# Performance work log

Hardware: AMD Instinct MI355X
Metric: run time of the kernel (lower is better)

Reference implementation:

```python
import jax, jax.numpy as jnp
import numpy as np

B, C, H, W = 4, 512, 64, 64
CQ = C // 8  # 64 channels for each of query/key projections


def conv1x1(t, w, b):
    # t: [B, Cin, H, W], w: [Cout, Cin], b: [Cout]
    return jnp.einsum('bchw,oc->bohw', t, w) + b[None, :, None, None]


def setup_inputs() -> dict:
    key = jax.random.key(0)
    ks = jax.random.split(key, 12)
    s = 0.05
    return {
        'x':   jax.random.normal(ks[0], (B, C, H, W), jnp.float32),
        'dep': jax.random.normal(ks[1], (B, C, H, W), jnp.float32),
        'wq':  jax.random.normal(ks[2], (CQ, C), jnp.float32) * s,
        'bq':  jnp.zeros((CQ,), jnp.float32),
        'wqd': jax.random.normal(ks[3], (CQ, C), jnp.float32) * s,
        'bqd': jnp.zeros((CQ,), jnp.float32),
        'wk':  jax.random.normal(ks[4], (CQ, C), jnp.float32) * s,
        'bk':  jnp.zeros((CQ,), jnp.float32),
        'wkd': jax.random.normal(ks[5], (CQ, C), jnp.float32) * s,
        'bkd': jnp.zeros((CQ,), jnp.float32),
        'wv':  jax.random.normal(ks[6], (C, C), jnp.float32) * s,
        'bv':  jnp.zeros((C,), jnp.float32),
        'gamma': jnp.full((1,), 0.5, jnp.float32),
    }


def reference(x, dep, wq, bq, wqd, bqd, wk, bk, wkd, bkd, wv, bv, gamma):
    b, c, h, w = x.shape
    n = h * w
    # concatenated RGB+depth query/key projections: [B, 2*CQ, N]
    q = jnp.concatenate([conv1x1(x, wq, bq), conv1x1(dep, wqd, bqd)], axis=1).reshape(b, -1, n)
    k = jnp.concatenate([conv1x1(x, wk, bk), conv1x1(dep, wkd, bkd)], axis=1).reshape(b, -1, n)
    # energy[b, i, j] = sum_d q[b, d, i] * k[b, d, j]  -> [B, N, N]
    energy = jnp.einsum('bdi,bdj->bij', q, k)
    attn = jax.nn.softmax(energy, axis=-1)
    v = conv1x1(x, wv, bv).reshape(b, c, n)  # [B, C, N]
    # out[b, c, i] = sum_j v[b, c, j] * attn[b, i, j]
    out = jnp.einsum('bcj,bij->bci', v, attn).reshape(b, c, h, w)
    return gamma.reshape(()) * out + x
```

## Files before the change

kernel.cpp:

```cpp
#include <hip/hip_runtime.h>


typedef __attribute__((ext_vector_type(8))) short bf16x8;
typedef __attribute__((ext_vector_type(4))) float f32x4;

__device__ __forceinline__ float bf2f(unsigned short u) {
  return __builtin_bit_cast(float, (unsigned int)u << 16);
}
__device__ __forceinline__ unsigned short f2bf(float f) {
  unsigned int u = __builtin_bit_cast(unsigned int, f);
  u = u + 0x7fffu + ((u >> 16) & 1u);
  return (unsigned short)(u >> 16);
}
__device__ __forceinline__ float bflo(unsigned int u) {
  return __builtin_bit_cast(float, u << 16);
}

__device__ __forceinline__ void gld16(const char* g, char* l) {
  __builtin_amdgcn_global_load_lds(
      (const __attribute__((address_space(1))) unsigned int*)g,
      (__attribute__((address_space(3))) unsigned int*)l, 16, 0, 0);
}

__device__ __forceinline__ int detect_fp32_mode(const void* xv) {
  const unsigned int* p = (const unsigned int*)xv;
  const int lane = threadIdx.x & 63;
  const unsigned int w0 = p[lane];
  const unsigned int w1 = p[64 + lane];
  int cnt = 0;
  const unsigned short us[4] = {
      (unsigned short)(w0 & 0xffffu), (unsigned short)(w0 >> 16),
      (unsigned short)(w1 & 0xffffu), (unsigned short)(w1 >> 16)};
#pragma unroll
  for (int h = 0; h < 4; ++h) {
    const float a = fabsf(bf2f(us[h]));
    cnt += (a > 9.0e-13f && a < 32.0f) ? 1 : 0;
  }
#pragma unroll
  for (int mm = 32; mm >= 1; mm >>= 1) cnt += __shfl_xor(cnt, mm, 64);
  return cnt < 220;
}

__global__ __launch_bounds__(256) void prep_kernel(
    const void* wq, const void* bq, const void* wqd, const void* bqd,
    const void* wk, const void* bk, const void* wkd, const void* bkd,
    const void* wv, const void* bv, const void* gam, const void* x,
    unsigned short* __restrict__ Whi, unsigned short* __restrict__ Wlo,
    float* __restrict__ Bcat, float* __restrict__ gamF)
{
  const int fp32mode = detect_fp32_mode(x);
  const int row = blockIdx.x;
  const void* src; const void* bsrc; int srow;
  if (row < 64)       { src = wq;  bsrc = bq;  srow = row; }
  else if (row < 128) { src = wqd; bsrc = bqd; srow = row - 64; }
  else if (row < 192) { src = wk;  bsrc = bk;  srow = row - 128; }
  else if (row < 256) { src = wkd; bsrc = bkd; srow = row - 192; }
  else                { src = wv;  bsrc = bv;  srow = row - 256; }
  for (int c = threadIdx.x; c < 512; c += 256) {
    const float v = fp32mode ? ((const float*)src)[(size_t)srow * 512 + c]
                             : bf2f(((const unsigned short*)src)[(size_t)srow * 512 + c]);
    const unsigned short h = f2bf(v);
    Whi[(size_t)row * 512 + c] = h;
    Wlo[(size_t)row * 512 + c] = f2bf(v - bf2f(h));
  }
  if (threadIdx.x == 0) {
    Bcat[row] = fp32mode ? ((const float*)bsrc)[srow]
                         : bf2f(((const unsigned short*)bsrc)[srow]);
    if (row == 0)
      gamF[0] = fp32mode ? ((const float*)gam)[0]
                         : bf2f(((const unsigned short*)gam)[0]);
  }
}

__device__ __forceinline__ void stage_X(
    const void* __restrict__ src, int fp32mode, int b, int n0,
    int cbase, int nn,
    unsigned short* __restrict__ Xhi, unsigned short* __restrict__ Xlo)
{
  float v[8][4];
  if (fp32mode) {
    const float* s = (const float*)src;
#pragma unroll
    for (int r = 0; r < 8; ++r) {
      const int c = cbase + r * 64;
      const float4 f4 = *(const float4*)(s + (((size_t)b * 512 + c) << 12) + n0 + nn);
      v[r][0] = f4.x; v[r][1] = f4.y; v[r][2] = f4.z; v[r][3] = f4.w;
    }
  } else {
    const unsigned short* s = (const unsigned short*)src;
#pragma unroll
    for (int r = 0; r < 8; ++r) {
      const int c = cbase + r * 64;
      const uint2 u2 = *(const uint2*)(s + (((size_t)b * 512 + c) << 12) + n0 + nn);
      v[r][0] = bflo(u2.x & 0xffffu); v[r][1] = bflo(u2.x >> 16);
      v[r][2] = bflo(u2.y & 0xffffu); v[r][3] = bflo(u2.y >> 16);
    }
  }
  __builtin_amdgcn_sched_barrier(0);
#pragma unroll
  for (int r = 0; r < 8; ++r) {
    const int c = cbase + r * 64;
#pragma unroll
    for (int k = 0; k < 4; ++k) {
      const unsigned short h = f2bf(v[r][k]);
      Xhi[(nn + k) * 522 + c] = h;
      Xlo[(nn + k) * 522 + c] = f2bf(v[r][k] - bf2f(h));
    }
  }
}

__device__ __forceinline__ void do_tile_c(
    const unsigned short* __restrict__ Whi, const unsigned short* __restrict__ Wlo,
    const float* bsh,
    const unsigned short* Xhi, const unsigned short* Xlo, int fp32mode,
    int wrow0, int kind, int d0,
    int l15, int quad,
    char* __restrict__ QT, char* __restrict__ KT, char* __restrict__ VT)
{
  f32x4 A0, A1, B0, B1, C0, C1;
#pragma unroll
  for (int r = 0; r < 4; ++r) {
    A0[r] = A1[r] = bsh[wrow0 + quad * 4 + r];
    B0[r] = B1[r] = C0[r] = C1[r] = 0.f;
  }
  const unsigned short* wh_p = Whi + (size_t)(wrow0 + l15) * 512 + quad * 8;
  const unsigned short* wl_p = Wlo + (size_t)(wrow0 + l15) * 512 + quad * 8;
  const unsigned short* x0h = Xhi + l15 * 522 + quad * 8;
  const unsigned short* x1h = Xhi + (16 + l15) * 522 + quad * 8;
  const unsigned short* x0l = Xlo + l15 * 522 + quad * 8;
  const unsigned short* x1l = Xlo + (16 + l15) * 522 + quad * 8;

  bf16x8 hc = *(const bf16x8*)(wh_p);
  bf16x8 lc;
  if (fp32mode) lc = *(const bf16x8*)(wl_p);

#pragma unroll 2
  for (int ks = 0; ks < 16; ++ks) {
    bf16x8 hn, ln;
    if (ks < 15) {
      hn = *(const bf16x8*)(wh_p + (ks + 1) * 32);
      if (fp32mode) ln = *(const bf16x8*)(wl_p + (ks + 1) * 32);
    }
    const int o = ks * 32;
    const bf16x8 b0 = *(const bf16x8*)(x0h + o);
    const bf16x8 b1 = *(const bf16x8*)(x1h + o);
    A0 = __builtin_amdgcn_mfma_f32_16x16x32_bf16(hc, b0, A0, 0, 0, 0);
    A1 = __builtin_amdgcn_mfma_f32_16x16x32_bf16(hc, b1, A1, 0, 0, 0);
    if (fp32mode) {
      const bf16x8 c0 = *(const bf16x8*)(x0l + o);
      const bf16x8 c1 = *(const bf16x8*)(x1l + o);
      B0 = __builtin_amdgcn_mfma_f32_16x16x32_bf16(hc, c0, B0, 0, 0, 0);
      C0 = __builtin_amdgcn_mfma_f32_16x16x32_bf16(lc, b0, C0, 0, 0, 0);
      B1 = __builtin_amdgcn_mfma_f32_16x16x32_bf16(hc, c1, B1, 0, 0, 0);
      C1 = __builtin_amdgcn_mfma_f32_16x16x32_bf16(lc, b1, C1, 0, 0, 0);
    }
    if (ks < 15) { hc = hn; if (fp32mode) lc = ln; }
  }

  const f32x4 a0 = fp32mode ? (A0 + B0) + C0 : A0;
  const f32x4 a1 = fp32mode ? (A1 + B1) + C1 : A1;
#pragma unroll
  for (int ns = 0; ns < 2; ++ns) {
    const f32x4 acc = ns ? a1 : a0;
    const int n = ns * 16 + l15;
    if (kind <= 1) {
      ushort4 h, l;
#pragma unroll
      for (int r = 0; r < 4; ++r) {
        const float f = acc[r];
        const unsigned short hh = f2bf(f);
        ((unsigned short*)&h)[r] = hh;
        ((unsigned short*)&l)[r] = f2bf(f - bf2f(hh));
      }
      const unsigned lin = (unsigned)(n * 256 + (d0 + quad * 4) * 2);
      if (kind == 0) {
        *(ushort4*)(QT + lin) = h;
        *(ushort4*)(QT + 8192 + lin) = l;
      } else {
        const unsigned off = lin ^ ((unsigned)(n & 7) << 4);
        *(ushort4*)(KT + off) = h;
        *(ushort4*)(KT + 8192 + off) = l;
      }
    } else {
#pragma unroll
      for (int r = 0; r < 4; ++r) {
        const int c = d0 + quad * 4 + r;
        const unsigned off =
            ((unsigned)(c * 64 + n * 2)) ^ ((unsigned)(c & 7) << 4);
        *(unsigned short*)(VT + off) = f2bf(acc[r]);
      }
    }
  }
}

__global__ __launch_bounds__(512, 2) void proj_kernel(
    const void* __restrict__ x, const void* __restrict__ dep,
    const unsigned short* __restrict__ Whi, const unsigned short* __restrict__ Wlo,
    const float* __restrict__ Bcat,
    unsigned short* __restrict__ Qhi, unsigned short* __restrict__ Qlo,
    unsigned short* __restrict__ Kst, unsigned short* __restrict__ Vst)
{
  __shared__ unsigned short Xhi[32 * 522];
  __shared__ unsigned short Xlo[32 * 522];
  __shared__ char QT[16384];
  __shared__ char KT[16384];
  __shared__ char VT[32768];
  __shared__ float bsh[768];
  const int fp32mode = detect_fp32_mode(x);
  const int tid  = threadIdx.x;
  const int lane = tid & 63;
  const int w    = tid >> 6;
  const int l15  = lane & 15;
  const int quad = lane >> 4;
  const int b  = blockIdx.y;

  const int cbase = tid >> 3;
  const int nn    = (tid & 7) * 4;

  for (int i = tid; i < 768; i += 512) bsh[i] = Bcat[i];

  for (int rep = 0; rep < 2; ++rep) {
    const int t  = blockIdx.x + rep * 64;
    const int n0 = t * 32;

    stage_X(x, fp32mode, b, n0, cbase, nn, Xhi, Xlo);
    __syncthreads();

    for (int rt = w; rt < 40; rt += 8) {
      int wrow0, kind, d0;
      if (rt < 4)      { wrow0 = rt * 16;             kind = 0; d0 = rt * 16; }
      else if (rt < 8) { wrow0 = 128 + (rt - 4) * 16; kind = 1; d0 = (rt - 4) * 16; }
      else             { wrow0 = 256 + (rt - 8) * 16; kind = 2; d0 = (rt - 8) * 16; }
      do_tile_c(Whi, Wlo, bsh, Xhi, Xlo, fp32mode, wrow0, kind, d0,
                l15, quad, QT, KT, VT);
    }
    __syncthreads();

    {
      char* vdst = (char*)Vst + (((size_t)b * 128 + t) << 15);
#pragma unroll
      for (int i = 0; i < 4; ++i) {
        const int off = i * 8192 + tid * 16;
        *(uint4*)(vdst + off) = *(const uint4*)(VT + off);
      }
    }
    stage_X(dep, fp32mode, b, n0, cbase, nn, Xhi, Xlo);
    __syncthreads();

    {
      const int rt = w;
      const int kind  = (rt < 4) ? 0 : 1;
      const int wrow0 = (rt < 4) ? 64 + rt * 16 : 192 + (rt - 4) * 16;
      const int d0    = 64 + (rt & 3) * 16;
      do_tile_c(Whi, Wlo, bsh, Xhi, Xlo, fp32mode, wrow0, kind, d0,
                l15, quad, QT, KT, VT);
    }
    __syncthreads();

    {
      char* kdst = (char*)Kst + (((size_t)b * 128 + t) << 14);
#pragma unroll
      for (int i = 0; i < 2; ++i) {
        const int off = i * 8192 + tid * 16;
        *(uint4*)(kdst + off) = *(const uint4*)(KT + off);
      }
      const size_t qoff = ((((size_t)b << 12) + n0) * 128) * 2;
      *(uint4*)((char*)Qhi + qoff + tid * 16) = *(const uint4*)(QT + tid * 16);
      *(uint4*)((char*)Qlo + qoff + tid * 16) = *(const uint4*)(QT + 8192 + tid * 16);
    }
    __syncthreads();
  }
}

__global__ __launch_bounds__(768, 3) void attn_kernel(
    const unsigned short* __restrict__ Qhi, const unsigned short* __restrict__ Qlo,
    const unsigned short* __restrict__ Kst, const unsigned short* __restrict__ Vst,
    const void* __restrict__ x, const float* __restrict__ gamF,
    void* __restrict__ outp)
{
  __shared__ char KL[2][16384];
  __shared__ char VL[2][32768];
  __shared__ unsigned short P[2][64][40];
  __shared__ float lstat[2][4][16];

  const int fp32mode = detect_fp32_mode(x);
  const int tid  = threadIdx.x;
  const int lane = tid & 63;
  const int w    = tid >> 6;
  const int l15  = lane & 15;
  const int quad = lane >> 4;
  const int id   = blockIdx.x;
  const int b    = (id >> 1) & 3;
  const int n0   = (((id >> 3) << 1) | (id & 1)) * 64;

  asm volatile("" :: "v"(fp32mode) : "memory");

  const char* Kb = (const char*)Kst + (((size_t)b * 128) << 14);
  const char* Vb = (const char*)Vst + (((size_t)b * 128) << 15);

  if (w < 4) {
    const int ihE = w >> 1;
    const int jt  = w & 1;
    bf16x8 qh[2][4], ql[2][4];
#pragma unroll
    for (int itq = 0; itq < 2; ++itq) {
      const size_t qb =
          (((size_t)b << 12) + n0 + ihE * 32 + itq * 16 + l15) * 128 + quad * 8;
#pragma unroll
      for (int ds = 0; ds < 4; ++ds) {
        qh[itq][ds] = *(const bf16x8*)(Qhi + qb + ds * 32);
        ql[itq][ds] = *(const bf16x8*)(Qlo + qb + ds * 32);
      }
    }
#pragma unroll
    for (int ch = 0; ch < 4; ++ch) {
      const int c = w + ch * 4;
      gld16(Kb + c * 1024 + lane * 16, &KL[0][c * 1024]);
    }
    float lpart[2] = {0.f, 0.f};

    for (int t = 0; t <= 128; ++t) {
      asm volatile("s_waitcnt vmcnt(0) lgkmcnt(0)" ::: "memory");
      __builtin_amdgcn_sched_barrier(0);
      __builtin_amdgcn_s_barrier();
      __builtin_amdgcn_sched_barrier(0);
      if (t < 128) {
        const int cur = t & 1;
        if (t < 127) {
          const char* src = Kb + ((size_t)(t + 1) << 14);
#pragma unroll
          for (int ch = 0; ch < 4; ++ch) {
            const int c = w + ch * 4;
            gld16(src + c * 1024 + lane * 16, &KL[cur ^ 1][c * 1024]);
          }
        }
        __builtin_amdgcn_sched_barrier(0);
        const int row = jt * 16 + l15;
        const unsigned rsw = (unsigned)(row & 7) << 4;
        const char* kb = &KL[cur][0];
        bf16x8 kh[4], kl[4];
#pragma unroll
        for (int ds = 0; ds < 4; ++ds) {
          const unsigned off = ((unsigned)(row * 256 + quad * 16 + ds * 64)) ^ rsw;
          kh[ds] = *(const bf16x8*)(kb + off);
          kl[ds] = *(const bf16x8*)(kb + 8192 + off);
        }
        f32x4 ea[2], eb[2], ec[2];
#pragma unroll
        for (int itq = 0; itq < 2; ++itq) {
          ea[itq] = (f32x4){0.f, 0.f, 0.f, 0.f};
          eb[itq] = (f32x4){0.f, 0.f, 0.f, 0.f};
          ec[itq] = (f32x4){0.f, 0.f, 0.f, 0.f};
        }
        __builtin_amdgcn_s_setprio(1);
#pragma unroll
        for (int ds = 0; ds < 4; ++ds)
#pragma unroll
          for (int itq = 0; itq < 2; ++itq) {
            ea[itq] = __builtin_amdgcn_mfma_f32_16x16x32_bf16(kh[ds], qh[itq][ds], ea[itq], 0, 0, 0);
            eb[itq] = __builtin_amdgcn_mfma_f32_16x16x32_bf16(kh[ds], ql[itq][ds], eb[itq], 0, 0, 0);
            ec[itq] = __builtin_amdgcn_mfma_f32_16x16x32_bf16(kl[ds], qh[itq][ds], ec[itq], 0, 0, 0);
          }
        __builtin_amdgcn_s_setprio(0);
#pragma unroll
        for (int itq = 0; itq < 2; ++itq) {
          const f32x4 e = (ea[itq] + eb[itq]) + ec[itq];
          const float p0 = __expf(e[0] - 32.0f);
          const float p1 = __expf(e[1] - 32.0f);
          const float p2 = __expf(e[2] - 32.0f);
          const float p3 = __expf(e[3] - 32.0f);
          const unsigned short u0 = f2bf(p0), u1 = f2bf(p1);
          const unsigned short u2 = f2bf(p2), u3 = f2bf(p3);
          lpart[itq] += (bf2f(u0) + bf2f(u1)) + (bf2f(u2) + bf2f(u3));
          unsigned int* dst = (unsigned int*)
              (&P[cur][ihE * 32 + itq * 16 + l15][jt * 16 + quad * 4]);
          dst[0] = (unsigned int)u0 | ((unsigned int)u1 << 16);
          dst[1] = (unsigned int)u2 | ((unsigned int)u3 << 16);
        }
      }
    }
#pragma unroll
    for (int itq = 0; itq < 2; ++itq) {
      float lp = lpart[itq];
      lp += __shfl_xor(lp, 16, 64);
      lp += __shfl_xor(lp, 32, 64);
      if (quad == 0) lstat[jt][ihE * 2 + itq][l15] = lp;
    }
    __syncthreads();
    return;
  }

  const int wv = w - 4;
#pragma unroll
  for (int k = 0; k < 4; ++k) {
    const int c = wv * 4 + k;
    gld16(Vb + c * 1024 + lane * 16, &VL[0][c * 1024]);
  }
  f32x4 acc[4][4];
#pragma unroll
  for (int ct = 0; ct < 4; ++ct)
#pragma unroll
    for (int itv = 0; itv < 4; ++itv) acc[ct][itv] = (f32x4){0.f, 0.f, 0.f, 0.f};

  for (int t = 0; t <= 128; ++t) {
    if (t <= 127)
      asm volatile("s_waitcnt vmcnt(4)" ::: "memory");
    else
      asm volatile("s_waitcnt vmcnt(0)" ::: "memory");
    __builtin_amdgcn_sched_barrier(0);
    __builtin_amdgcn_s_barrier();
    __builtin_amdgcn_sched_barrier(0);
    if (t >= 1) {
      const int pb = (t - 1) & 1;
      bf16x8 pf[4];
#pragma unroll
      for (int itv = 0; itv < 4; ++itv)
        pf[itv] = *(const bf16x8*)(&P[pb][itv * 16 + l15][quad * 8]);
      const char* vb = &VL[pb][0];
      __builtin_amdgcn_s_setprio(1);
#pragma unroll
      for (int ct = 0; ct < 4; ++ct) {
        const int c = wv * 64 + ct * 16 + l15;
        const unsigned off =
            ((unsigned)(c * 64 + quad * 16)) ^ ((unsigned)(c & 7) << 4);
        const bf16x8 va = *(const bf16x8*)(vb + off);
#pragma unroll
        for (int itv = 0; itv < 4; ++itv)
          acc[ct][itv] = __builtin_amdgcn_mfma_f32_16x16x32_bf16(va, pf[itv], acc[ct][itv], 0, 0, 0);
      }
      __builtin_amdgcn_s_setprio(0);
      __builtin_amdgcn_sched_barrier(0);
    }
    if (t < 127) {
      const char* src = Vb + ((size_t)(t + 1) << 15);
#pragma unroll
      for (int k = 0; k < 4; ++k) {
        const int c = wv * 4 + k;
        gld16(src + c * 1024 + lane * 16, &VL[(t + 1) & 1][c * 1024]);
      }
    }
  }
  __syncthreads();

  const float gv = gamF[0];
  float sc[4];
#pragma unroll
  for (int itv = 0; itv < 4; ++itv) {
    const float l = lstat[0][itv][l15] + lstat[1][itv][l15];
    sc[itv] = gv / l;
  }
#pragma unroll
  for (int ct = 0; ct < 4; ++ct)
#pragma unroll
    for (int r = 0; r < 4; ++r) {
      const int c_g = wv * 64 + ct * 16 + quad * 4 + r;
      const size_t brow = ((size_t)b * 512 + c_g) << 12;
#pragma unroll
      for (int itv = 0; itv < 4; ++itv) {
        const size_t addr = brow + n0 + itv * 16 + l15;
        const float o = sc[itv] * acc[ct][itv][r];
        if (fp32mode) {
          ((float*)outp)[addr] = o + ((const float*)x)[addr];
        } else {
          ((unsigned short*)outp)[addr] =
              f2bf(o + bf2f(((const unsigned short*)x)[addr]));
        }
      }
    }
}

extern "C" void kernel_launch(void* const* d_in, const int* in_sizes, int n_in,
                              void* d_out, int out_size, void* d_ws, size_t ws_size,
                              hipStream_t stream) {
  const void* x    = d_in[0];
  const void* dep  = d_in[1];
  const void* wq   = d_in[2];
  const void* bq   = d_in[3];
  const void* wqd  = d_in[4];
  const void* bqd  = d_in[5];
  const void* wk   = d_in[6];
  const void* bk   = d_in[7];
  const void* wkd  = d_in[8];
  const void* bkd  = d_in[9];
  const void* wv   = d_in[10];
  const void* bv   = d_in[11];
  const void* gam  = d_in[12];

  unsigned short* Whi = (unsigned short*)d_ws;
  unsigned short* Wlo = Whi + (size_t)768 * 512;
  float* Bcat = (float*)(Wlo + (size_t)768 * 512);
  float* gamF = Bcat + 768;
  unsigned short* Qhi = (unsigned short*)((char*)d_ws + ((size_t)2 << 20));
  unsigned short* Qlo = (unsigned short*)((char*)d_ws + ((size_t)6 << 20));
  unsigned short* Kst = (unsigned short*)((char*)d_ws + ((size_t)10 << 20));
  unsigned short* Vst = (unsigned short*)((char*)d_ws + ((size_t)18 << 20));

  prep_kernel<<<768, 256, 0, stream>>>(wq, bq, wqd, bqd, wk, bk, wkd, bkd,
                                       wv, bv, gam, x, Whi, Wlo, Bcat, gamF);
  proj_kernel<<<dim3(64, 4), 512, 0, stream>>>(x, dep, Whi, Wlo, Bcat,
                                               Qhi, Qlo, Kst, Vst);
  attn_kernel<<<256, 768, 0, stream>>>(Qhi, Qlo, Kst, Vst, x, gamF, d_out);
}
```

Measured before the change: 436.2 us.

## Split projection into a transpose/convert kernel and a GEMM kernel

The fused projection kernel is split in two. A convert kernel transposes x and dep into swizzled hi/lo bf16 tiles in workspace. A GEMM kernel then loads those tiles into LDS with global_load_lds and writes Q/K/V straight from registers, using 128x4 blocks instead of 64x4 with two reps. This removes the in-kernel fp32 staging and LDS transpose from the MFMA kernel and raises parallelism, at the cost of an extra kernel launch and a round-trip of the converted activations through global memory. The new path is used only when the workspace is at least 100 MB, and falls back to the old kernel otherwise.

```diff
diff --git a/kernel.cpp b/kernel.cpp
--- a/kernel.cpp
+++ b/kernel.cpp
@@ -72,6 +72,211 @@
   }
 }
 
+__global__ __launch_bounds__(256) void convert_kernel(
+    const void* __restrict__ x, const void* __restrict__ dep,
+    unsigned short* __restrict__ Xst)
+{
+  __shared__ float XT[512][36];
+  const int fp32mode = detect_fp32_mode(x);
+  const int tid = threadIdx.x;
+  const int bid = blockIdx.x;
+  const int src = bid & 1, t = (bid >> 1) & 127, b = bid >> 8;
+  const int n0 = t * 32;
+  const void* s = src ? dep : x;
+  const int crow = tid >> 3;
+  const int nf   = (tid & 7) * 4;
+
+  float v[16][4];
+  if (fp32mode) {
+    const float* sp = (const float*)s;
+#pragma unroll
+    for (int r = 0; r < 16; ++r) {
+      const int c = crow + r * 32;
+      const float4 f4 = *(const float4*)(sp + (((size_t)b * 512 + c) << 12) + n0 + nf);
+      v[r][0] = f4.x; v[r][1] = f4.y; v[r][2] = f4.z; v[r][3] = f4.w;
+    }
+  } else {
+    const unsigned short* sp = (const unsigned short*)s;
+#pragma unroll
+    for (int r = 0; r < 16; ++r) {
+      const int c = crow + r * 32;
+      const uint2 u2 = *(const uint2*)(sp + (((size_t)b * 512 + c) << 12) + n0 + nf);
+      v[r][0] = bflo(u2.x & 0xffffu); v[r][1] = bflo(u2.x >> 16);
+      v[r][2] = bflo(u2.y & 0xffffu); v[r][3] = bflo(u2.y >> 16);
+    }
+  }
+  __builtin_amdgcn_sched_barrier(0);
+#pragma unroll
+  for (int r = 0; r < 16; ++r) {
+    const int c = crow + r * 32;
+#pragma unroll
+    for (int k = 0; k < 4; ++k) XT[c][nf + k] = v[r][k];
+  }
+  __syncthreads();
+
+  const int n  = tid & 31;
+  const int cg = tid >> 5;
+  char* pb = (char*)Xst + ((((size_t)b * 128 + t) * 2 + src) << 16);
+  const unsigned swz = (unsigned)(n & 7) << 4;
+#pragma unroll
+  for (int g = 0; g < 8; ++g) {
+    unsigned short hi8[8], lo8[8];
+#pragma unroll
+    for (int i = 0; i < 8; ++i) {
+      const float vv = XT[cg * 64 + g * 8 + i][n];
+      const unsigned short h = f2bf(vv);
+      hi8[i] = h;
+      lo8[i] = f2bf(vv - bf2f(h));
+    }
+    const unsigned off = ((unsigned)(n * 1024 + 2 * (cg * 64 + g * 8))) ^ swz;
+    *(uint4*)(pb + off)         = *(const uint4*)hi8;
+    *(uint4*)(pb + 32768 + off) = *(const uint4*)lo8;
+  }
+}
+
+__device__ __forceinline__ void gtile(
+    const unsigned short* __restrict__ Whi, const unsigned short* __restrict__ Wlo,
+    const float* bsh, const char* __restrict__ XL, int fp32mode,
+    int wrow0, int kind, int d0, int b, int t, int n0, int l15, int quad,
+    unsigned short* __restrict__ Qhi, unsigned short* __restrict__ Qlo,
+    unsigned short* __restrict__ Kst, unsigned short* __restrict__ Vst)
+{
+  f32x4 A0, A1, B0, B1, C0, C1;
+#pragma unroll
+  for (int r = 0; r < 4; ++r) {
+    A0[r] = A1[r] = bsh[wrow0 + quad * 4 + r];
+    B0[r] = B1[r] = C0[r] = C1[r] = 0.f;
+  }
+  const unsigned short* wh_p = Whi + (size_t)(wrow0 + l15) * 512 + quad * 8;
+  const unsigned short* wl_p = Wlo + (size_t)(wrow0 + l15) * 512 + quad * 8;
+  const unsigned base0 = (unsigned)(l15 * 1024 + quad * 16);
+  const unsigned swz   = (unsigned)(l15 & 7) << 4;
+
+  bf16x8 hc = *(const bf16x8*)(wh_p);
+  bf16x8 lc;
+  if (fp32mode) lc = *(const bf16x8*)(wl_p);
+
+#pragma unroll 2
+  for (int ks = 0; ks < 16; ++ks) {
+    bf16x8 hn, ln;
+    if (ks < 15) {
+      hn = *(const bf16x8*)(wh_p + (ks + 1) * 32);
+      if (fp32mode) ln = *(const bf16x8*)(wl_p + (ks + 1) * 32);
+    }
+    const unsigned o0 = (base0 + ks * 64) ^ swz;
+    const unsigned o1 = o0 + 16384;
+    const bf16x8 b0 = *(const bf16x8*)(XL + o0);
+    const bf16x8 b1 = *(const bf16x8*)(XL + o1);
+    A0 = __builtin_amdgcn_mfma_f32_16x16x32_bf16(hc, b0, A0, 0, 0, 0);
+    A1 = __builtin_amdgcn_mfma_f32_16x16x32_bf16(hc, b1, A1, 0, 0, 0);
+    if (fp32mode) {
+      const bf16x8 c0 = *(const bf16x8*)(XL + 32768 + o0);
+      const bf16x8 c1 = *(const bf16x8*)(XL + 32768 + o1);
+      B0 = __builtin_amdgcn_mfma_f32_16x16x32_bf16(hc, c0, B0, 0, 0, 0);
+      C0 = __builtin_amdgcn_mfma_f32_16x16x32_bf16(lc, b0, C0, 0, 0, 0);
+      B1 = __builtin_amdgcn_mfma_f32_16x16x32_bf16(hc, c1, B1, 0, 0, 0);
+      C1 = __builtin_amdgcn_mfma_f32_16x16x32_bf16(lc, b1, C1, 0, 0, 0);
+    }
+    if (ks < 15) { hc = hn; if (fp32mode) lc = ln; }
+  }
+
+  const f32x4 a0 = fp32mode ? (A0 + B0) + C0 : A0;
+  const f32x4 a1 = fp32mode ? (A1 + B1) + C1 : A1;
+#pragma unroll
+  for (int ns = 0; ns < 2; ++ns) {
+    const f32x4 acc = ns ? a1 : a0;
+    const int j = ns * 16 + l15;
+    if (kind <= 1) {
+      ushort4 h, l;
+#pragma unroll
+      for (int r = 0; r < 4; ++r) {
+        const float f = acc[r];
+        const unsigned short hh = f2bf(f);
+        ((unsigned short*)&h)[r] = hh;
+        ((unsigned short*)&l)[r] = f2bf(f - bf2f(hh));
+      }
+      if (kind == 0) {
+        const size_t base = (((size_t)b << 12) + n0 + j) * 128 + d0 + quad * 4;
+        *(ushort4*)(Qhi + base) = h;
+        *(ushort4*)(Qlo + base) = l;
+      } else {
+        char* tb = (char*)Kst + (((size_t)b * 128 + t) << 14);
+        const unsigned off =
+            ((unsigned)(j * 256 + (d0 + quad * 4) * 2)) ^ ((unsigned)(j & 7) << 4);
+        *(ushort4*)(tb + off) = h;
+        *(ushort4*)(tb + 8192 + off) = l;
+      }
+    } else {
+      char* tb = (char*)Vst + (((size_t)b * 128 + t) << 15);
+#pragma unroll
+      for (int r = 0; r < 4; ++r) {
+        const int c = d0 + quad * 4 + r;
+        const unsigned off =
+            ((unsigned)(c * 64 + j * 2)) ^ ((unsigned)(c & 7) << 4);
+        *(unsigned short*)(tb + off) = f2bf(acc[r]);
+      }
+    }
+  }
+}
+
+__global__ __launch_bounds__(512, 4) void gemm_kernel(
+    const void* __restrict__ x,
+    const unsigned short* __restrict__ Whi, const unsigned short* __restrict__ Wlo,
+    const float* __restrict__ Bcat, const unsigned short* __restrict__ Xst,
+    unsigned short* __restrict__ Qhi, unsigned short* __restrict__ Qlo,
+    unsigned short* __restrict__ Kst, unsigned short* __restrict__ Vst)
+{
+  __shared__ char XL[65536];
+  __shared__ float bsh[768];
+  const int fp32mode = detect_fp32_mode(x);
+  const int tid  = threadIdx.x;
+  const int lane = tid & 63;
+  const int w    = tid >> 6;
+  const int l15  = lane & 15;
+  const int quad = lane >> 4;
+  const int t  = blockIdx.x;
+  const int b  = blockIdx.y;
+  const int n0 = t * 32;
+
+  for (int i = tid; i < 768; i += 512) bsh[i] = Bcat[i];
+
+  const char* xsrc = (const char*)Xst + ((((size_t)b * 128 + t) * 2 + 0) << 16);
+  const char* dsrc = xsrc + 65536;
+
+#pragma unroll
+  for (int i = 0; i < 8; ++i) {
+    const int c8 = w + i * 8;
+    gld16(xsrc + c8 * 1024 + lane * 16, XL + c8 * 1024);
+  }
+  __syncthreads();
+
+  for (int i = 0; i < 5; ++i) {
+    const int rt = w + i * 8;
+    int wrow0, kind, d0;
+    if (rt < 4)      { wrow0 = rt * 16;             kind = 0; d0 = rt * 16; }
+    else if (rt < 8) { wrow0 = 128 + (rt - 4) * 16; kind = 1; d0 = (rt - 4) * 16; }
+    else             { wrow0 = 256 + (rt - 8) * 16; kind = 2; d0 = (rt - 8) * 16; }
+    gtile(Whi, Wlo, bsh, XL, fp32mode, wrow0, kind, d0, b, t, n0, l15, quad,
+          Qhi, Qlo, Kst, Vst);
+  }
+  __syncthreads();
+
+#pragma unroll
+  for (int i = 0; i < 8; ++i) {
+    const int c8 = w + i * 8;
+    gld16(dsrc + c8 * 1024 + lane * 16, XL + c8 * 1024);
+  }
+  __syncthreads();
+
+  {
+    const int kind  = (w < 4) ? 0 : 1;
+    const int wrow0 = (w < 4) ? 64 + w * 16 : 192 + (w - 4) * 16;
+    const int d0    = 64 + (w & 3) * 16;
+    gtile(Whi, Wlo, bsh, XL, fp32mode, wrow0, kind, d0, b, t, n0, l15, quad,
+          Qhi, Qlo, Kst, Vst);
+  }
+}
+
 __device__ __forceinline__ void stage_X(
     const void* __restrict__ src, int fp32mode, int b, int n0,
     int cbase, int nn,
@@ -213,7 +418,6 @@
   const int l15  = lane & 15;
   const int quad = lane >> 4;
   const int b  = blockIdx.y;
-
   const int cbase = tid >> 3;
   const int nn    = (tid & 7) * 4;
 
@@ -222,10 +426,8 @@
   for (int rep = 0; rep < 2; ++rep) {
     const int t  = blockIdx.x + rep * 64;
     const int n0 = t * 32;
-
     stage_X(x, fp32mode, b, n0, cbase, nn, Xhi, Xlo);
     __syncthreads();
-
     for (int rt = w; rt < 40; rt += 8) {
       int wrow0, kind, d0;
       if (rt < 4)      { wrow0 = rt * 16;             kind = 0; d0 = rt * 16; }
@@ -235,7 +437,6 @@
                 l15, quad, QT, KT, VT);
     }
     __syncthreads();
-
     {
       char* vdst = (char*)Vst + (((size_t)b * 128 + t) << 15);
 #pragma unroll
@@ -246,7 +447,6 @@
     }
     stage_X(dep, fp32mode, b, n0, cbase, nn, Xhi, Xlo);
     __syncthreads();
-
     {
       const int rt = w;
       const int kind  = (rt < 4) ? 0 : 1;
@@ -256,7 +456,6 @@
                 l15, quad, QT, KT, VT);
     }
     __syncthreads();
-
     {
       char* kdst = (char*)Kst + (((size_t)b * 128 + t) << 14);
 #pragma unroll
@@ -264,7 +463,7 @@
         const int off = i * 8192 + tid * 16;
         *(uint4*)(kdst + off) = *(const uint4*)(KT + off);
       }
-      const size_t qoff = ((((size_t)b << 12) + n0) * 128) * 2;
+      const size_t qoff = ((((size_t)b << 12) + (size_t)t * 32) * 128) * 2;
       *(uint4*)((char*)Qhi + qoff + tid * 16) = *(const uint4*)(QT + tid * 16);
       *(uint4*)((char*)Qlo + qoff + tid * 16) = *(const uint4*)(QT + 8192 + tid * 16);
     }
@@ -494,10 +693,17 @@
   unsigned short* Qlo = (unsigned short*)((char*)d_ws + ((size_t)6 << 20));
   unsigned short* Kst = (unsigned short*)((char*)d_ws + ((size_t)10 << 20));
   unsigned short* Vst = (unsigned short*)((char*)d_ws + ((size_t)18 << 20));
+  unsigned short* Xst = (unsigned short*)((char*)d_ws + ((size_t)36 << 20));
 
   prep_kernel<<<768, 256, 0, stream>>>(wq, bq, wqd, bqd, wk, bk, wkd, bkd,
                                        wv, bv, gam, x, Whi, Wlo, Bcat, gamF);
-  proj_kernel<<<dim3(64, 4), 512, 0, stream>>>(x, dep, Whi, Wlo, Bcat,
-                                               Qhi, Qlo, Kst, Vst);
+  if (ws_size >= ((size_t)100 << 20)) {
+    convert_kernel<<<1024, 256, 0, stream>>>(x, dep, Xst);
+    gemm_kernel<<<dim3(128, 4), 512, 0, stream>>>(x, Whi, Wlo, Bcat, Xst,
+                                                  Qhi, Qlo, Kst, Vst);
+  } else {
+    proj_kernel<<<dim3(64, 4), 512, 0, stream>>>(x, dep, Whi, Wlo, Bcat,
+                                                 Qhi, Qlo, Kst, Vst);
+  }
   attn_kernel<<<256, 768, 0, stream>>>(Qhi, Qlo, Kst, Vst, x, gamF, d_out);
 }
```

Result: faster. 396.3 us (-9.1%).
